# Kernel tuning notes

Measured on AMD Instinct MI355X. Metric: run time of the kernel, lower is better.

## Reference

```python
import jax, jax.numpy as jnp
import numpy as np
from jax import lax

T = 2048          # tokens (batch*seq, module flattens to [-1, hidden])
H = 2048          # hidden_size
E = 32            # n_routed_experts
DF = 1024         # moe_intermediate_size
DS = 4096         # moe_shared_expert_intermediate_size
TOP_K = 6         # num_experts_per_tok
N_GROUP = 8
TOPK_GROUP = 4
SCALE = 2.5       # routed_scaling_factor
NORM_TOPK = True


def relu2(x):
    r = jax.nn.relu(x)
    return r * r


def setup_inputs() -> dict:
    key = jax.random.key(0)
    ks = jax.random.split(key, 7)
    s = 0.02
    return {
        "x": jax.random.normal(ks[0], (T, H), dtype=jnp.float32),
        "router_w": jax.random.normal(ks[1], (E, H), dtype=jnp.float32) * s,
        "router_b": jax.random.normal(ks[2], (E,), dtype=jnp.float32) * s,
        "w_up": jax.random.normal(ks[3], (E, H, DF), dtype=jnp.float32) * s,
        "w_down": jax.random.normal(ks[4], (E, DF, H), dtype=jnp.float32) * s,
        "shared_up": jax.random.normal(ks[5], (H, DS), dtype=jnp.float32) * s,
        "shared_down": jax.random.normal(ks[6], (DS, H), dtype=jnp.float32) * s,
    }


def _route(x, router_w, router_b):
    # router in fp32: logits -> sigmoid scores -> group-restricted top-k
    logits = x @ router_w.T                                  # [T, E]
    scores = jax.nn.sigmoid(logits)
    sfc = scores + router_b[None, :]                         # scores_for_choice
    gsize = E // N_GROUP
    grp = sfc.reshape(T, N_GROUP, gsize)
    group_scores = lax.top_k(grp, 2)[0].sum(-1)              # [T, n_group] sum of top-2
    _, gidx = lax.top_k(group_scores, TOPK_GROUP)            # [T, topk_group]
    group_mask = jax.nn.one_hot(gidx, N_GROUP, dtype=sfc.dtype).sum(1)  # [T, n_group]
    score_mask = jnp.repeat(group_mask, gsize, axis=1)       # [T, E]
    masked = jnp.where(score_mask > 0, sfc, 0.0)
    _, tidx = lax.top_k(masked, TOP_K)                       # [T, top_k]
    tw = jnp.take_along_axis(scores, tidx, axis=1)           # gather raw scores
    if NORM_TOPK:
        tw = tw / (tw.sum(-1, keepdims=True) + 1e-20)
    tw = tw * SCALE
    return tidx, tw


def reference(x, router_w, router_b, w_up, w_down, shared_up, shared_down):
    tidx, tw = _route(x, router_w, router_b)
    # dense combine weights [T, E]; equals sum of routed weights per expert
    combine = (jax.nn.one_hot(tidx, E, dtype=tw.dtype) * tw[..., None]).sum(1)
    # routed experts (no bias, so scaling before down_proj == scaling the output)
    h = jnp.einsum('td,edf->tef', x, w_up)                   # [T, E, DF]
    a = relu2(h) * combine[:, :, None]
    moe_out = jnp.einsum('tef,efd->td', a, w_down)           # [T, H]
    shared_out = relu2(x @ shared_up) @ shared_down
    return moe_out + shared_out
```

## Files before the change

kernel.cpp:

```cpp
#include <hip/hip_runtime.h>
#include <hip/hip_bf16.h>
#include <math.h>

#define T_TOK 2048
#define HID   2048
#define NE    32
#define DF    1024
#define DSZ   4096
#define TOPK  6
#define NGRP  8
#define TOPKG 4
#define RSCALE 2.5f
#define EXT_E 36
#define NSLOT 20480

typedef __attribute__((ext_vector_type(8))) short short8;
typedef __attribute__((ext_vector_type(4))) short short4v;
typedef __attribute__((ext_vector_type(4))) float f32x4;

typedef __attribute__((address_space(1))) const void gv1;
typedef __attribute__((address_space(3))) void lv3;

static __device__ __forceinline__ void gload16(const void* g, void* l) {
    __builtin_amdgcn_global_load_lds((gv1*)g, (lv3*)l, 16, 0, 0);
}

static __device__ __forceinline__ unsigned short f2b(float f) {
    union { float f; unsigned u; } v; v.f = f;
    unsigned r = v.u + 0x7fffu + ((v.u >> 16) & 1u);
    return (unsigned short)(r >> 16);
}

static __device__ __forceinline__ unsigned short b16(float f) {
    union { __hip_bfloat16 h; unsigned short u; } c;
    c.h = __float2bfloat16(f);
    return c.u;
}

static __device__ __forceinline__ float b2f(unsigned short b) {
    union { float f; unsigned u; } v; v.u = ((unsigned)b) << 16;
    return v.f;
}

__global__ __launch_bounds__(256)
void router_kernel(const float* __restrict__ x, const float* __restrict__ rw,
                   const float* __restrict__ rb,
                   int* __restrict__ tidx, float* __restrict__ tw,
                   int* __restrict__ counts, unsigned short* __restrict__ xb) {
    __shared__ float xs[HID];
    __shared__ float part[256];
    __shared__ float scores[NE];
    __shared__ float sfc[NE];
    int t = blockIdx.x;
    int tid = threadIdx.x;
    for (int i = tid; i < HID / 4; i += 256) {
        ((float4*)xs)[i] = ((const float4*)(x + (size_t)t * HID))[i];
    }
    __syncthreads();
    {
        float4 a = ((const float4*)xs)[tid * 2];
        float4 b = ((const float4*)xs)[tid * 2 + 1];
        short8 o;
        o[0] = (short)f2b(a.x); o[1] = (short)f2b(a.y); o[2] = (short)f2b(a.z); o[3] = (short)f2b(a.w);
        o[4] = (short)f2b(b.x); o[5] = (short)f2b(b.y); o[6] = (short)f2b(b.z); o[7] = (short)f2b(b.w);
        *(short8*)(xb + (size_t)t * HID + tid * 8) = o;
    }
    int e = tid & 31, ch = tid >> 5;
    const float* w = rw + (size_t)e * HID + ch * 256;
    const float* xv = xs + ch * 256;
    float p = 0.f;
    #pragma unroll 8
    for (int k = 0; k < 256; ++k) p += xv[k] * w[k];
    part[tid] = p;
    __syncthreads();
    if (tid < 32) {
        float l = 0.f;
        #pragma unroll
        for (int c = 0; c < 8; ++c) l += part[c * 32 + tid];
        float s = 1.f / (1.f + expf(-l));
        scores[tid] = s;
        sfc[tid] = s + rb[tid];
    }
    __syncthreads();
    if (tid == 0) {
        float gs[NGRP];
        for (int g = 0; g < NGRP; ++g) {
            float v[4];
            for (int i = 0; i < 4; ++i) v[i] = sfc[g * 4 + i];
            int bi = 0;
            for (int i = 1; i < 4; ++i) if (v[i] > v[bi]) bi = i;
            float m1 = v[bi]; v[bi] = -INFINITY;
            int bj = 0;
            for (int i = 1; i < 4; ++i) if (v[i] > v[bj]) bj = i;
            gs[g] = m1 + v[bj];
        }
        bool gsel[NGRP];
        for (int g = 0; g < NGRP; ++g) gsel[g] = false;
        for (int k = 0; k < TOPKG; ++k) {
            int bi = -1; float b = -INFINITY;
            for (int g = 0; g < NGRP; ++g)
                if (!gsel[g] && gs[g] > b) { b = gs[g]; bi = g; }
            gsel[bi] = true;
        }
        float masked[NE];
        for (int i = 0; i < NE; ++i) masked[i] = gsel[i >> 2] ? sfc[i] : 0.0f;
        int sel[TOPK]; float wv[TOPK]; float wsum = 0.f;
        for (int k = 0; k < TOPK; ++k) {
            int bi = -1; float b = -INFINITY;
            for (int i = 0; i < NE; ++i)
                if (masked[i] > b) { b = masked[i]; bi = i; }
            masked[bi] = -INFINITY;
            sel[k] = bi; wv[k] = scores[bi]; wsum += wv[k];
        }
        float inv = RSCALE / (wsum + 1e-20f);
        for (int k = 0; k < TOPK; ++k) {
            tidx[t * TOPK + k] = sel[k];
            tw[t * TOPK + k] = wv[k] * inv;
            atomicAdd(&counts[sel[k]], 1);
        }
    }
}

__global__ void scan_kernel(const int* __restrict__ counts, int* __restrict__ offsets) {
    if (threadIdx.x == 0) {
        int a = 0;
        for (int e2 = 0; e2 < NE; ++e2) { offsets[e2] = a; a += counts[e2]; }
        offsets[NE] = a;
        for (int j = 1; j <= 4; ++j) offsets[NE + j] = 12288 + j * T_TOK;
    }
}

__global__ void scatter_kernel(const int* __restrict__ tidx, const float* __restrict__ tw,
                               const int* __restrict__ offsets, int* __restrict__ cursors,
                               int* __restrict__ perm, float* __restrict__ pw,
                               int* __restrict__ slot_of) {
    int t = blockIdx.x * blockDim.x + threadIdx.x;
    if (t >= T_TOK) return;
    for (int k = 0; k < TOPK; ++k) {
        int e = tidx[t * TOPK + k];
        int pos = atomicAdd(&cursors[e], 1);
        int slot = offsets[e] + pos;
        perm[slot] = t;
        pw[slot] = tw[t * TOPK + k];
        slot_of[t * TOPK + k] = slot;
    }
    #pragma unroll
    for (int j = 0; j < 4; ++j) {
        int slot = 12288 + j * T_TOK + t;
        perm[slot] = t;
        pw[slot] = 1.0f;
    }
}

template<int MODE>
__global__ __launch_bounds__(256, 2)
void gemm_tr_kernel(const unsigned short* __restrict__ Abuf,
                    const float* __restrict__ Wmain, const float* __restrict__ Wsh,
                    unsigned short* __restrict__ Cbuf, const int* __restrict__ offsets,
                    const int* __restrict__ perm, const float* __restrict__ pw) {
    constexpr int K = (MODE == 0) ? HID : DF;
    constexpr int N = (MODE == 0) ? DF : HID;
    __shared__ __align__(16) char lds[32768];
    char* As = lds;
    char* Bs = lds + 16384;

    int tid = threadIdx.x;
    int lane = tid & 63, wvid = tid >> 6, wr = wvid >> 1, wc = wvid & 1;

    int bz = blockIdx.z;
    int off = offsets[bz], end = offsets[bz + 1];
    int row0 = off + blockIdx.y * 128;
    if (row0 >= end) return;
    int n0 = blockIdx.x * 128;

    const float* Bsrc; long ldb;
    if (MODE == 0) {
        if (bz < NE) { Bsrc = Wmain + (size_t)bz * HID * DF; ldb = DF; }
        else         { Bsrc = Wsh + (size_t)(bz - NE) * DF;  ldb = DSZ; }
    } else {
        Bsrc = (bz < NE) ? (Wmain + (size_t)bz * DF * HID)
                         : (Wsh + (size_t)(bz - NE) * DF * HID);
        ldb = HID;
    }

    int lr = lane >> 3;
    int csrc = (((lane & 7) ^ lr) << 4);
    size_t abyte[4];
    int ldsoff[4];
    #pragma unroll
    for (int p = 0; p < 4; ++p) {
        int r = p * 32 + wvid * 8 + lr;
        int gr = row0 + r;
        if (gr > end - 1) gr = end - 1;
        int s = (MODE == 0) ? perm[gr] : gr;
        abyte[p] = (size_t)s * (K * 2);
        ldsoff[p] = (p * 32 + wvid * 8) * 128;
    }

    int kr0 = (tid & 3) + ((tid >> 6) & 1) * 4;
    int nc  = ((tid >> 2) & 15) * 4 + (tid >> 7) * 64;
    int bwbase = (kr0 >> 2) * 1024 + (nc >> 4) * 128 + (kr0 & 3) * 32 + (nc & 15) * 2;

    unsigned bsb = (unsigned)(uintptr_t)(lv3*)Bs + (unsigned)((lane >> 4) * 2048 + (lane & 15) * 8);

    f32x4 acc[4][4] = {};
    for (int k0 = 0; k0 < K; k0 += 64) {
        __syncthreads();
        #pragma unroll
        for (int p = 0; p < 4; ++p)
            gload16((const char*)Abuf + abyte[p] + k0 * 2 + csrc, As + ldsoff[p]);
        {
            const float* bp = Bsrc + (size_t)(k0 + kr0) * ldb + n0 + nc;
            #pragma unroll
            for (int p = 0; p < 8; ++p) {
                float4 v = *(const float4*)(bp + (size_t)p * 8 * ldb);
                unsigned short h[4] = { b16(v.x), b16(v.y), b16(v.z), b16(v.w) };
                *(short4v*)(Bs + bwbase + p * 2048) = *(short4v*)h;
            }
        }
        __syncthreads();
        #pragma unroll
        for (int ks = 0; ks < 2; ++ks) {
            int r16 = lane & 15, kg = lane >> 4;
            short8 af[4];
            #pragma unroll
            for (int m = 0; m < 4; ++m) {
                int r = wr * 64 + m * 16 + r16;
                af[m] = *(const short8*)(As + r * 128 + ((ks * 64 + kg * 16) ^ ((r & 7) << 4)));
            }
            short4v t0[4], t1[4];
            #pragma unroll
            for (int n = 0; n < 4; ++n) {
                unsigned a = bsb + ks * 8192 + (wc * 4 + n) * 128;
                asm volatile("ds_read_b64_tr_b16 %0, %2\n\t"
                             "ds_read_b64_tr_b16 %1, %2 offset:1024"
                             : "=v"(t0[n]), "=v"(t1[n]) : "v"(a));
            }
            asm volatile("s_waitcnt lgkmcnt(0)" ::: "memory");
            __builtin_amdgcn_sched_barrier(0);
            #pragma unroll
            for (int n = 0; n < 4; ++n) {
                short8 bfr;
                bfr[0] = t0[n][0]; bfr[1] = t0[n][1]; bfr[2] = t0[n][2]; bfr[3] = t0[n][3];
                bfr[4] = t1[n][0]; bfr[5] = t1[n][1]; bfr[6] = t1[n][2]; bfr[7] = t1[n][3];
                #pragma unroll
                for (int m = 0; m < 4; ++m)
                    acc[m][n] = __builtin_amdgcn_mfma_f32_16x16x32_bf16(af[m], bfr, acc[m][n], 0, 0, 0);
            }
        }
    }

    int r16 = lane & 15, rg = lane >> 4;
    #pragma unroll
    for (int m = 0; m < 4; ++m) {
        #pragma unroll
        for (int j = 0; j < 4; ++j) {
            int rr = row0 + wr * 64 + m * 16 + rg * 4 + j;
            if (rr < end) {
                if (MODE == 0) {
                    float scale = pw[rr];
                    #pragma unroll
                    for (int n = 0; n < 4; ++n) {
                        int cc = n0 + wc * 64 + n * 16 + r16;
                        float v = acc[m][n][j];
                        v = v > 0.f ? v * v : 0.f;
                        Cbuf[(size_t)rr * N + cc] = f2b(v * scale);
                    }
                } else {
                    #pragma unroll
                    for (int n = 0; n < 4; ++n) {
                        int cc = n0 + wc * 64 + n * 16 + r16;
                        Cbuf[(size_t)rr * N + cc] = f2b(acc[m][n][j]);
                    }
                }
            }
        }
    }
}

__global__ void combine_kernel(const unsigned short* __restrict__ slotout,
                               const int* __restrict__ slot_of,
                               float* __restrict__ out) {
    int t = blockIdx.x, tid = threadIdx.x;
    int s[10];
    #pragma unroll
    for (int k = 0; k < TOPK; ++k) s[k] = slot_of[t * TOPK + k];
    #pragma unroll
    for (int j = 0; j < 4; ++j) s[TOPK + j] = 12288 + j * T_TOK + t;
    int c = tid * 8;
    float a[8] = {0.f, 0.f, 0.f, 0.f, 0.f, 0.f, 0.f, 0.f};
    #pragma unroll
    for (int k = 0; k < 10; ++k) {
        short8 v = *(const short8*)(slotout + (size_t)s[k] * HID + c);
        #pragma unroll
        for (int i = 0; i < 8; ++i) a[i] += b2f((unsigned short)v[i]);
    }
    *(float4*)(out + (size_t)t * HID + c) = make_float4(a[0], a[1], a[2], a[3]);
    *(float4*)(out + (size_t)t * HID + c + 4) = make_float4(a[4], a[5], a[6], a[7]);
}

extern "C" void kernel_launch(void* const* d_in, const int* in_sizes, int n_in,
                              void* d_out, int out_size, void* d_ws, size_t ws_size,
                              hipStream_t stream) {
    const float* x     = (const float*)d_in[0];
    const float* rw    = (const float*)d_in[1];
    const float* rb    = (const float*)d_in[2];
    const float* w_up  = (const float*)d_in[3];
    const float* w_dn  = (const float*)d_in[4];
    const float* sh_up = (const float*)d_in[5];
    const float* sh_dn = (const float*)d_in[6];
    float* out = (float*)d_out;
    char* ws = (char*)d_ws;

    int*   counts  = (int*)(ws);
    int*   cursors = (int*)(ws + 128);
    int*   offsets = (int*)(ws + 256);
    int*   tidx    = (int*)(ws + 1024);
    float* tw      = (float*)(ws + 50176);
    int*   slot_of = (int*)(ws + 99328);
    int*   perm    = (int*)(ws + 148480);
    float* pw      = (float*)(ws + 230400);
    unsigned short* xb   = (unsigned short*)(ws + 312320);
    unsigned short* act  = (unsigned short*)(ws + 8700928);
    unsigned short* slotout = (unsigned short*)(ws + 50643968);

    hipMemsetAsync(ws, 0, 256, stream);

    router_kernel<<<T_TOK, 256, 0, stream>>>(x, rw, rb, tidx, tw, counts, xb);
    scan_kernel<<<1, 64, 0, stream>>>(counts, offsets);
    scatter_kernel<<<(T_TOK + 255) / 256, 256, 0, stream>>>(tidx, tw, offsets, cursors,
                                                            perm, pw, slot_of);

    gemm_tr_kernel<0><<<dim3(DF / 128, T_TOK / 128, EXT_E), 256, 0, stream>>>(
        xb, w_up, sh_up, act, offsets, perm, pw);

    gemm_tr_kernel<1><<<dim3(HID / 128, T_TOK / 128, EXT_E), 256, 0, stream>>>(
        act, w_dn, sh_dn, slotout, offsets, perm, pw);

    combine_kernel<<<T_TOK, 256, 0, stream>>>(slotout, slot_of, out);
}
```

Before: 680.6 us.

## Pre-convert weights to bf16 and load B tiles via direct global-to-LDS

Adds a separate kernel that converts all expert and shared weights from fp32 to bf16 once per call into workspace. The GEMM B-tile load then uses async global_load_lds of bf16 data instead of per-thread fp32 loads, conversion and LDS stores. This removes repeated conversion work and halves the B bytes each tile reads. In exchange it adds a full pass that reads about 600MB of fp32 weights and writes about 300MB of bf16, every call.

```diff
diff --git a/kernel.cpp b/kernel.cpp
--- a/kernel.cpp
+++ b/kernel.cpp
@@ -29,12 +29,6 @@
     union { float f; unsigned u; } v; v.f = f;
     unsigned r = v.u + 0x7fffu + ((v.u >> 16) & 1u);
     return (unsigned short)(r >> 16);
-}
-
-static __device__ __forceinline__ unsigned short b16(float f) {
-    union { __hip_bfloat16 h; unsigned short u; } c;
-    c.h = __float2bfloat16(f);
-    return c.u;
 }
 
 static __device__ __forceinline__ float b2f(unsigned short b) {
@@ -152,10 +146,29 @@
     }
 }
 
+__global__ __launch_bounds__(256)
+void cvt_weights_kernel(const float* __restrict__ w_up, const float* __restrict__ w_dn,
+                        const float* __restrict__ sh_up, const float* __restrict__ sh_dn,
+                        unsigned short* __restrict__ wupb, unsigned short* __restrict__ wdnb,
+                        unsigned short* __restrict__ shupb, unsigned short* __restrict__ shdnb) {
+    size_t c = (size_t)blockIdx.x * 256 + threadIdx.x;
+    const float* src; unsigned short* dst; size_t off;
+    if (c < 8388608ull)        { src = w_up;  dst = wupb;  off = c; }
+    else if (c < 16777216ull)  { src = w_dn;  dst = wdnb;  off = c - 8388608ull; }
+    else if (c < 17825792ull)  { src = sh_up; dst = shupb; off = c - 16777216ull; }
+    else                       { src = sh_dn; dst = shdnb; off = c - 17825792ull; }
+    float4 a = ((const float4*)src)[off * 2];
+    float4 b = ((const float4*)src)[off * 2 + 1];
+    short8 o;
+    o[0] = (short)f2b(a.x); o[1] = (short)f2b(a.y); o[2] = (short)f2b(a.z); o[3] = (short)f2b(a.w);
+    o[4] = (short)f2b(b.x); o[5] = (short)f2b(b.y); o[6] = (short)f2b(b.z); o[7] = (short)f2b(b.w);
+    *(short8*)(dst + off * 8) = o;
+}
+
 template<int MODE>
 __global__ __launch_bounds__(256, 2)
 void gemm_tr_kernel(const unsigned short* __restrict__ Abuf,
-                    const float* __restrict__ Wmain, const float* __restrict__ Wsh,
+                    const unsigned short* __restrict__ Wmain, const unsigned short* __restrict__ Wsh,
                     unsigned short* __restrict__ Cbuf, const int* __restrict__ offsets,
                     const int* __restrict__ perm, const float* __restrict__ pw) {
     constexpr int K = (MODE == 0) ? HID : DF;
@@ -173,20 +186,20 @@
     if (row0 >= end) return;
     int n0 = blockIdx.x * 128;
 
-    const float* Bsrc; long ldb;
+    const unsigned short* Bsrc; long ldbb;
     if (MODE == 0) {
-        if (bz < NE) { Bsrc = Wmain + (size_t)bz * HID * DF; ldb = DF; }
-        else         { Bsrc = Wsh + (size_t)(bz - NE) * DF;  ldb = DSZ; }
+        if (bz < NE) { Bsrc = Wmain + (size_t)bz * HID * DF; ldbb = DF; }
+        else         { Bsrc = Wsh + (size_t)(bz - NE) * DF;  ldbb = DSZ; }
     } else {
         Bsrc = (bz < NE) ? (Wmain + (size_t)bz * DF * HID)
                          : (Wsh + (size_t)(bz - NE) * DF * HID);
-        ldb = HID;
+        ldbb = HID;
     }
 
     int lr = lane >> 3;
     int csrc = (((lane & 7) ^ lr) << 4);
     size_t abyte[4];
-    int ldsoff[4];
+    int ldsA[4];
     #pragma unroll
     for (int p = 0; p < 4; ++p) {
         int r = p * 32 + wvid * 8 + lr;
@@ -194,29 +207,30 @@
         if (gr > end - 1) gr = end - 1;
         int s = (MODE == 0) ? perm[gr] : gr;
         abyte[p] = (size_t)s * (K * 2);
-        ldsoff[p] = (p * 32 + wvid * 8) * 128;
-    }
-
-    int kr0 = (tid & 3) + ((tid >> 6) & 1) * 4;
-    int nc  = ((tid >> 2) & 15) * 4 + (tid >> 7) * 64;
-    int bwbase = (kr0 >> 2) * 1024 + (nc >> 4) * 128 + (kr0 & 3) * 32 + (nc & 15) * 2;
+        ldsA[p] = (p * 32 + wvid * 8) * 128;
+    }
+
+    int bk = (lane >> 1) & 3;
+    int bn = (lane >> 3) * 16 + (lane & 1) * 8;
+    size_t bbyte[4];
+    int ldsB[4];
+    #pragma unroll
+    for (int p = 0; p < 4; ++p) {
+        int kg = wvid + 4 * p;
+        bbyte[p] = ((size_t)(kg * 4 + bk) * ldbb + n0 + bn) * 2;
+        ldsB[p] = kg * 1024;
+    }
 
     unsigned bsb = (unsigned)(uintptr_t)(lv3*)Bs + (unsigned)((lane >> 4) * 2048 + (lane & 15) * 8);
 
     f32x4 acc[4][4] = {};
     for (int k0 = 0; k0 < K; k0 += 64) {
+        size_t kbB = (size_t)k0 * (ldbb * 2);
         __syncthreads();
         #pragma unroll
-        for (int p = 0; p < 4; ++p)
-            gload16((const char*)Abuf + abyte[p] + k0 * 2 + csrc, As + ldsoff[p]);
-        {
-            const float* bp = Bsrc + (size_t)(k0 + kr0) * ldb + n0 + nc;
-            #pragma unroll
-            for (int p = 0; p < 8; ++p) {
-                float4 v = *(const float4*)(bp + (size_t)p * 8 * ldb);
-                unsigned short h[4] = { b16(v.x), b16(v.y), b16(v.z), b16(v.w) };
-                *(short4v*)(Bs + bwbase + p * 2048) = *(short4v*)h;
-            }
+        for (int p = 0; p < 4; ++p) {
+            gload16((const char*)Abuf + abyte[p] + k0 * 2 + csrc, As + ldsA[p]);
+            gload16((const char*)Bsrc + kbB + bbyte[p], Bs + ldsB[p]);
         }
         __syncthreads();
         #pragma unroll
@@ -320,9 +334,13 @@
     int*   slot_of = (int*)(ws + 99328);
     int*   perm    = (int*)(ws + 148480);
     float* pw      = (float*)(ws + 230400);
-    unsigned short* xb   = (unsigned short*)(ws + 312320);
-    unsigned short* act  = (unsigned short*)(ws + 8700928);
+    unsigned short* xb      = (unsigned short*)(ws + 312320);
+    unsigned short* act     = (unsigned short*)(ws + 8700928);
     unsigned short* slotout = (unsigned short*)(ws + 50643968);
+    unsigned short* wupb    = (unsigned short*)(ws + 134530048);
+    unsigned short* wdnb    = (unsigned short*)(ws + 268747776);
+    unsigned short* shupb   = (unsigned short*)(ws + 402965504);
+    unsigned short* shdnb   = (unsigned short*)(ws + 419742720);
 
     hipMemsetAsync(ws, 0, 256, stream);
 
@@ -331,11 +349,14 @@
     scatter_kernel<<<(T_TOK + 255) / 256, 256, 0, stream>>>(tidx, tw, offsets, cursors,
                                                             perm, pw, slot_of);
 
+    cvt_weights_kernel<<<73728, 256, 0, stream>>>(w_up, w_dn, sh_up, sh_dn,
+                                                  wupb, wdnb, shupb, shdnb);
+
     gemm_tr_kernel<0><<<dim3(DF / 128, T_TOK / 128, EXT_E), 256, 0, stream>>>(
-        xb, w_up, sh_up, act, offsets, perm, pw);
+        xb, wupb, shupb, act, offsets, perm, pw);
 
     gemm_tr_kernel<1><<<dim3(HID / 128, T_TOK / 128, EXT_E), 256, 0, stream>>>(
-        act, w_dn, sh_dn, slotout, offsets, perm, pw);
+        act, wdnb, shdnb, slotout, offsets, perm, pw);
 
     combine_kernel<<<T_TOK, 256, 0, stream>>>(slotout, slot_of, out);
 }
```

New measurement: 596.7 us. 1.14x faster.
